# Kernel tuning notes

Hardware: AMD Instinct MI355X
Metric: run time of the kernel (lower is better)

## Reference

```python
import jax, jax.numpy as jnp
import numpy as np

ALPHA = 0.2  # LeakyReLU negative slope
NEG_INF = -9e15


def setup_inputs() -> dict:
    key = jax.random.key(0)
    k1, k2, k3, k4 = jax.random.split(key, 4)
    N, Fin, Fout = 8192, 256, 64
    h = jax.random.normal(k1, (N, Fin), dtype=jnp.float32)
    adj = jax.random.randint(k2, (N, N), 0, 2, dtype=jnp.int32)
    # xavier_uniform with gain=1.414
    def xavier(k, shape, gain=1.414):
        fan_in, fan_out = shape[0], shape[1]
        bound = gain * np.sqrt(6.0 / (fan_in + fan_out))
        return jax.random.uniform(k, shape, jnp.float32, -bound, bound)
    W = xavier(k3, (Fin, Fout))
    a = xavier(k4, (2 * Fout, 1))
    return {"h": h, "adj": adj, "W": W, "a": a}


def reference(h, adj, W, a):
    Fout = W.shape[1]
    Wh = h @ W                                  # [N, Fout]
    Wh1 = Wh @ a[:Fout, :]                      # [N, 1]
    Wh2 = Wh @ a[Fout:, :]                      # [N, 1]
    e = jax.nn.leaky_relu(Wh1 + Wh2.T, negative_slope=ALPHA)  # [N, N]
    attention = jnp.where(adj > 0, e, NEG_INF)
    attention = jax.nn.softmax(attention, axis=1)
    h_prime = attention @ Wh                    # [N, Fout]
    return jax.nn.elu(h_prime)
```

## Files before the change

### kernel.cpp

```cpp
#include <hip/hip_runtime.h>
#include <hip/hip_bf16.h>
#include <math.h>

#define NN 8192
#define FIN 256
#define FOUT 64
#define LRELU_ALPHA 0.2f
#define TI 16
#define TJ 256
#define JS 8
#define JCHUNK (NN / JS)

typedef __attribute__((ext_vector_type(8))) short short8v;
typedef __attribute__((ext_vector_type(4))) float f32x4;

static __device__ inline unsigned short f2bf(float f) {
  __hip_bfloat16 b = __float2bfloat16(f);
  return *reinterpret_cast<unsigned short*>(&b);
}


__global__ __launch_bounds__(256) void gat_prep(
    const float* __restrict__ W, const float* __restrict__ a,
    unsigned short* __restrict__ WF, float* __restrict__ wa1,
    float* __restrict__ wa2) {
  const int t = threadIdx.x;
  if (blockIdx.x < 8) {
    const int wid = blockIdx.x * 4 + (t >> 6);
    const int ks = wid >> 2, nt = wid & 3;
    const int l = t & 63;
    const int kg = l >> 4, nn = l & 15;
    unsigned short frag[8];
#pragma unroll
    for (int e = 0; e < 8; ++e) {
      frag[e] = f2bf(W[(ks * 32 + kg * 8 + e) * FOUT + nt * 16 + nn]);
    }
    *(short8v*)&WF[wid * 512 + l * 8] = *(short8v*)frag;
  } else {
    float s1 = 0.f, s2 = 0.f;
#pragma unroll 4
    for (int c = 0; c < FOUT; c += 4) {
      const float4 wv = *(const float4*)&W[t * FOUT + c];
      const float4 a1 = *(const float4*)&a[c];
      const float4 a2 = *(const float4*)&a[FOUT + c];
      s1 += wv.x * a1.x + wv.y * a1.y + wv.z * a1.z + wv.w * a1.w;
      s2 += wv.x * a2.x + wv.y * a2.y + wv.z * a2.z + wv.w * a2.w;
    }
    wa1[t] = s1;
    wa2[t] = s2;
  }
}

__global__ __launch_bounds__(256) void gat_wh5(
    const float* __restrict__ h, const unsigned short* __restrict__ WF,
    const float* __restrict__ wa1, const float* __restrict__ wa2,
    unsigned short* __restrict__ WhF, float* __restrict__ Wh1,
    float* __restrict__ Wh2) {
  __shared__ __align__(16) float hs[TI][260];

  const int t = threadIdx.x;
  const int i0 = blockIdx.x * TI;

#pragma unroll
  for (int q = 0; q < 4; ++q) {
    const int idx = q * 256 + t;
    const float4 v = *(const float4*)&h[(size_t)i0 * FIN + (size_t)idx * 4];
    const int row = idx >> 6, col = (idx & 63) * 4;
    *(float4*)&hs[row][col] = v;
  }
  __syncthreads();

  {
    const int row = t >> 4, s = t & 15;
    float p1 = 0.f, p2 = 0.f;
#pragma unroll
    for (int q = 0; q < 16; ++q) {
      const int k = s + q * 16;
      const float hv = hs[row][k];
      p1 = fmaf(hv, wa1[k], p1);
      p2 = fmaf(hv, wa2[k], p2);
    }
#pragma unroll
    for (int off = 8; off; off >>= 1) {
      p1 += __shfl_xor(p1, off);
      p2 += __shfl_xor(p2, off);
    }
    if (s == 0) {
      Wh1[i0 + row] = p1;
      Wh2[i0 + row] = p2;
    }
  }

  const int w = t >> 6, l = t & 63;
  const int kg = l >> 4, m = l & 15;
  f32x4 acc = {0.f, 0.f, 0.f, 0.f};
#pragma unroll
  for (int ks = 0; ks < 8; ++ks) {
    const float4 fa = *(const float4*)&hs[m][ks * 32 + kg * 8];
    const float4 fb = *(const float4*)&hs[m][ks * 32 + kg * 8 + 4];
    unsigned short af[8];
    af[0] = f2bf(fa.x); af[1] = f2bf(fa.y);
    af[2] = f2bf(fa.z); af[3] = f2bf(fa.w);
    af[4] = f2bf(fb.x); af[5] = f2bf(fb.y);
    af[6] = f2bf(fb.z); af[7] = f2bf(fb.w);
    const short8v bf = *(const short8v*)&WF[(ks * 4 + w) * 512 + l * 8];
    acc =
        __builtin_amdgcn_mfma_f32_16x16x32_bf16(*(short8v*)af, bf, acc, 0, 0, 0);
  }

  const int k0 = i0 + kg * 4;
  const int col = w * 16 + m;
  const int basef = ((k0 >> 5) * 4 + (col >> 4)) * 512 +
                    (((k0 >> 3) & 3) * 16 + (col & 15)) * 8 + (k0 & 7);
  ushort4 st;
  st.x = f2bf(acc[0]);
  st.y = f2bf(acc[1]);
  st.z = f2bf(acc[2]);
  st.w = f2bf(acc[3]);
  *(ushort4*)&WhF[basef] = st;
}

__global__ __launch_bounds__(256) void gat_attn6(
    const int* __restrict__ adj, const unsigned short* __restrict__ WhF,
    const float* __restrict__ Wh1, const float* __restrict__ Wh2,
    float* __restrict__ num, float* __restrict__ den) {
  __shared__ __align__(16) unsigned short p_lds[2][TI * TJ];
  __shared__ float den_lds[TI];

  const int t = threadIdx.x;
  const int jsplit = blockIdx.x & (JS - 1);
  const int i0 = (blockIdx.x >> 3) * TI;
  const int j0 = jsplit * JCHUNK;

  const int r0 = t >> 5;
  const int col8 = (t & 31) * 8;
  const float w1_0 = Wh1[i0 + r0];
  const float w1_1 = Wh1[i0 + r0 + 8];

  const int w = t >> 6;
  const int l = t & 63;
  const int arow = l & 15;
  const int kg = l >> 4;
  const int colw = w * 16 + arow;

  float ds0 = 0.f, ds1 = 0.f;
  f32x4 acc = {0.f, 0.f, 0.f, 0.f};

  const int wkt = (t & 31) >> 2, wkg = t & 3, wsw = t & 15;
  const int wr0 = wkt * 1024 + wkg * 256 + (((r0 ^ wsw) & 15) << 4);
  const int wr1 = wr0 ^ 128;

  int4 a00, a01, a10, a11;
  float4 w2a, w2b;
  {
    const int4* ap0 = (const int4*)&adj[(size_t)(i0 + r0) * NN + j0 + col8];
    const int4* ap1 = (const int4*)&adj[(size_t)(i0 + r0 + 8) * NN + j0 + col8];
    a00 = ap0[0]; a01 = ap0[1];
    a10 = ap1[0]; a11 = ap1[1];
    w2a = *(const float4*)&Wh2[j0 + col8];
    w2b = *(const float4*)&Wh2[j0 + col8 + 4];
  }

  for (int jb = j0, it = 0; jb < j0 + JCHUNK; jb += TJ, ++it) {
    unsigned short* pl = &p_lds[it & 1][0];

    const float w2v[8] = {w2a.x, w2a.y, w2a.z, w2a.w,
                          w2b.x, w2b.y, w2b.z, w2b.w};
    const int am0[8] = {a00.x, a00.y, a00.z, a00.w, a01.x, a01.y, a01.z, a01.w};
    const int am1[8] = {a10.x, a10.y, a10.z, a10.w, a11.x, a11.y, a11.z, a11.w};

    short8v pv0, pv1;
#pragma unroll
    for (int e = 0; e < 8; ++e) {
      float v0 = w1_0 + w2v[e];
      v0 = v0 > 0.f ? v0 : LRELU_ALPHA * v0;
      float p0 = (am0[e] > 0) ? __expf(v0) : 0.f;
      ds0 += p0;
      pv0[e] = (short)f2bf(p0);
      float v1 = w1_1 + w2v[e];
      v1 = v1 > 0.f ? v1 : LRELU_ALPHA * v1;
      float p1 = (am1[e] > 0) ? __expf(v1) : 0.f;
      ds1 += p1;
      pv1[e] = (short)f2bf(p1);
    }
    *(short8v*)((char*)pl + wr0) = pv0;
    *(short8v*)((char*)pl + wr1) = pv1;

    if (jb + TJ < j0 + JCHUNK) {
      const int jn = jb + TJ;
      const int4* ap0 = (const int4*)&adj[(size_t)(i0 + r0) * NN + jn + col8];
      const int4* ap1 =
          (const int4*)&adj[(size_t)(i0 + r0 + 8) * NN + jn + col8];
      a00 = ap0[0]; a01 = ap0[1];
      a10 = ap1[0]; a11 = ap1[1];
      w2a = *(const float4*)&Wh2[jn + col8];
      w2b = *(const float4*)&Wh2[jn + col8 + 4];
    }

    asm volatile("s_waitcnt lgkmcnt(0)" ::: "memory");
    __builtin_amdgcn_sched_barrier(0);
    __builtin_amdgcn_s_barrier();

    const int kblk0 = jb >> 5;
#pragma unroll
    for (int kt = 0; kt < 8; ++kt) {
      const int swk = (kt * 4 + kg) & 15;
      const int raddr = kt * 1024 + (kg << 8) + ((arow ^ swk) << 4);
      short8v af = *(const short8v*)((const char*)pl + raddr);
      short8v bf = *(const short8v*)&WhF[((kblk0 + kt) * 4 + w) * 512 + l * 8];
      acc = __builtin_amdgcn_mfma_f32_16x16x32_bf16(af, bf, acc, 0, 0, 0);
    }
  }

#pragma unroll
  for (int off = 16; off; off >>= 1) {
    ds0 += __shfl_xor(ds0, off);
    ds1 += __shfl_xor(ds1, off);
  }
  if ((t & 31) == 0) {
    const int rr = t >> 5;
    den_lds[rr] = ds0;
    den_lds[rr + 8] = ds1;
  }
  __syncthreads();
  if (t < TI) den[(size_t)jsplit * NN + i0 + t] = den_lds[t];

#pragma unroll
  for (int r = 0; r < 4; ++r) {
    num[((size_t)jsplit * NN + i0 + kg * 4 + r) * FOUT + colw] = acc[r];
  }
}

__global__ __launch_bounds__(256) void gat_comb(
    const float* __restrict__ num, const float* __restrict__ den,
    float* __restrict__ out) {
  const int idx = blockIdx.x * 256 + threadIdx.x;
  const int row = idx >> 6;
  float n = 0.f, d = 0.f;
#pragma unroll
  for (int s = 0; s < JS; ++s) {
    n += num[(size_t)s * NN * FOUT + idx];
    d += den[(size_t)s * NN + row];
  }
  float v = n / d;
  out[idx] = v > 0.f ? v : expm1f(v);
}

extern "C" void kernel_launch(void* const* d_in, const int* in_sizes, int n_in,
                              void* d_out, int out_size, void* d_ws,
                              size_t ws_size, hipStream_t stream) {
  const float* h = (const float*)d_in[0];
  const int* adj = (const int*)d_in[1];
  const float* W = (const float*)d_in[2];
  const float* a = (const float*)d_in[3];
  float* out = (float*)d_out;

  unsigned short* WhF = (unsigned short*)d_ws;
  float* Wh1 = (float*)((char*)d_ws + (1 << 20));
  float* Wh2 = Wh1 + NN;
  float* num = Wh2 + NN;
  float* den = num + (size_t)JS * NN * FOUT;
  unsigned short* WF = (unsigned short*)((char*)d_ws + (24u << 20));
  float* wa1 = (float*)((char*)d_ws + (24u << 20) + (64u << 10));
  float* wa2 = wa1 + FIN;

  gat_prep<<<9, 256, 0, stream>>>(W, a, WF, wa1, wa2);
  gat_wh5<<<NN / TI, 256, 0, stream>>>(h, WF, wa1, wa2, WhF, Wh1, Wh2);
  gat_attn6<<<(NN / TI) * JS, 256, 0, stream>>>(adj, WhF, Wh1, Wh2, num, den);
  gat_comb<<<NN * FOUT / 256, 256, 0, stream>>>(num, den, out);
}
```

Baseline: 80.19 us.

## Factor exp of LeakyReLU into per-node exponentials and fuse prep into Wh kernel

Precomputes exp(Wh1), exp(0.2*Wh1), exp(Wh2) and exp(0.2*Wh2) per node, so the attention inner loop forms each score as a product of two exponentials instead of evaluating an exp per pair. The sign test becomes a check of whether the product exceeds 1. The W fragment packing and W·a projection are folded into the Wh kernel, where every block recomputes them into shared memory, removing one launch. The cost is twice the Wh2-side loads per tile, redundant per-block prep work, and possible float overflow or underflow in the products, since no max subtraction is applied.

```diff
diff --git a/kernel.cpp b/kernel.cpp
--- a/kernel.cpp
+++ b/kernel.cpp
@@ -5,7 +5,6 @@
 #define NN 8192
 #define FIN 256
 #define FOUT 64
-#define LRELU_ALPHA 0.2f
 #define TI 16
 #define TJ 256
 #define JS 8
@@ -20,23 +19,43 @@
 }
 
 
-__global__ __launch_bounds__(256) void gat_prep(
-    const float* __restrict__ W, const float* __restrict__ a,
-    unsigned short* __restrict__ WF, float* __restrict__ wa1,
-    float* __restrict__ wa2) {
+__global__ __launch_bounds__(256) void gat_wh7(
+    const float* __restrict__ h, const float* __restrict__ W,
+    const float* __restrict__ a, unsigned short* __restrict__ WhF,
+    float* __restrict__ E1, float* __restrict__ F1, float* __restrict__ E2,
+    float* __restrict__ F2) {
+  __shared__ __align__(16) float hs[TI][260];
+  __shared__ __align__(16) unsigned short wfl[16384];
+  __shared__ float wal[2][FIN];
+
   const int t = threadIdx.x;
-  if (blockIdx.x < 8) {
-    const int wid = blockIdx.x * 4 + (t >> 6);
+  const int i0 = blockIdx.x * TI;
+
+#pragma unroll
+  for (int q = 0; q < 4; ++q) {
+    const int idx = q * 256 + t;
+    const float4 v = *(const float4*)&h[(size_t)i0 * FIN + (size_t)idx * 4];
+    const int row = idx >> 6, col = (idx & 63) * 4;
+    *(float4*)&hs[row][col] = v;
+  }
+
+  {
+    const int wid = t >> 3;
     const int ks = wid >> 2, nt = wid & 3;
-    const int l = t & 63;
-    const int kg = l >> 4, nn = l & 15;
-    unsigned short frag[8];
-#pragma unroll
-    for (int e = 0; e < 8; ++e) {
-      frag[e] = f2bf(W[(ks * 32 + kg * 8 + e) * FOUT + nt * 16 + nn]);
-    }
-    *(short8v*)&WF[wid * 512 + l * 8] = *(short8v*)frag;
-  } else {
+#pragma unroll
+    for (int li = 0; li < 8; ++li) {
+      const int l = (t & 7) * 8 + li;
+      const int kg = l >> 4, nn = l & 15;
+      unsigned short fr[8];
+#pragma unroll
+      for (int e = 0; e < 8; ++e) {
+        fr[e] = f2bf(W[(ks * 32 + kg * 8 + e) * FOUT + nt * 16 + nn]);
+      }
+      *(short8v*)&wfl[wid * 512 + l * 8] = *(short8v*)fr;
+    }
+  }
+
+  {
     float s1 = 0.f, s2 = 0.f;
 #pragma unroll 4
     for (int c = 0; c < FOUT; c += 4) {
@@ -46,27 +65,8 @@
       s1 += wv.x * a1.x + wv.y * a1.y + wv.z * a1.z + wv.w * a1.w;
       s2 += wv.x * a2.x + wv.y * a2.y + wv.z * a2.z + wv.w * a2.w;
     }
-    wa1[t] = s1;
-    wa2[t] = s2;
-  }
-}
-
-__global__ __launch_bounds__(256) void gat_wh5(
-    const float* __restrict__ h, const unsigned short* __restrict__ WF,
-    const float* __restrict__ wa1, const float* __restrict__ wa2,
-    unsigned short* __restrict__ WhF, float* __restrict__ Wh1,
-    float* __restrict__ Wh2) {
-  __shared__ __align__(16) float hs[TI][260];
-
-  const int t = threadIdx.x;
-  const int i0 = blockIdx.x * TI;
-
-#pragma unroll
-  for (int q = 0; q < 4; ++q) {
-    const int idx = q * 256 + t;
-    const float4 v = *(const float4*)&h[(size_t)i0 * FIN + (size_t)idx * 4];
-    const int row = idx >> 6, col = (idx & 63) * 4;
-    *(float4*)&hs[row][col] = v;
+    wal[0][t] = s1;
+    wal[1][t] = s2;
   }
   __syncthreads();
 
@@ -77,8 +77,8 @@
     for (int q = 0; q < 16; ++q) {
       const int k = s + q * 16;
       const float hv = hs[row][k];
-      p1 = fmaf(hv, wa1[k], p1);
-      p2 = fmaf(hv, wa2[k], p2);
+      p1 = fmaf(hv, wal[0][k], p1);
+      p2 = fmaf(hv, wal[1][k], p2);
     }
 #pragma unroll
     for (int off = 8; off; off >>= 1) {
@@ -86,8 +86,10 @@
       p2 += __shfl_xor(p2, off);
     }
     if (s == 0) {
-      Wh1[i0 + row] = p1;
-      Wh2[i0 + row] = p2;
+      E1[i0 + row] = __expf(p1);
+      F1[i0 + row] = __expf(0.2f * p1);
+      E2[i0 + row] = __expf(p2);
+      F2[i0 + row] = __expf(0.2f * p2);
     }
   }
 
@@ -103,7 +105,7 @@
     af[2] = f2bf(fa.z); af[3] = f2bf(fa.w);
     af[4] = f2bf(fb.x); af[5] = f2bf(fb.y);
     af[6] = f2bf(fb.z); af[7] = f2bf(fb.w);
-    const short8v bf = *(const short8v*)&WF[(ks * 4 + w) * 512 + l * 8];
+    const short8v bf = *(const short8v*)&wfl[(ks * 4 + w) * 512 + l * 8];
     acc =
         __builtin_amdgcn_mfma_f32_16x16x32_bf16(*(short8v*)af, bf, acc, 0, 0, 0);
   }
@@ -120,9 +122,10 @@
   *(ushort4*)&WhF[basef] = st;
 }
 
-__global__ __launch_bounds__(256) void gat_attn6(
+__global__ __launch_bounds__(256) void gat_attn7(
     const int* __restrict__ adj, const unsigned short* __restrict__ WhF,
-    const float* __restrict__ Wh1, const float* __restrict__ Wh2,
+    const float* __restrict__ E1, const float* __restrict__ F1,
+    const float* __restrict__ E2, const float* __restrict__ F2,
     float* __restrict__ num, float* __restrict__ den) {
   __shared__ __align__(16) unsigned short p_lds[2][TI * TJ];
   __shared__ float den_lds[TI];
@@ -134,8 +137,8 @@
 
   const int r0 = t >> 5;
   const int col8 = (t & 31) * 8;
-  const float w1_0 = Wh1[i0 + r0];
-  const float w1_1 = Wh1[i0 + r0 + 8];
+  const float e1_0 = E1[i0 + r0], f1_0 = F1[i0 + r0];
+  const float e1_1 = E1[i0 + r0 + 8], f1_1 = F1[i0 + r0 + 8];
 
   const int w = t >> 6;
   const int l = t & 63;
@@ -151,35 +154,41 @@
   const int wr1 = wr0 ^ 128;
 
   int4 a00, a01, a10, a11;
-  float4 w2a, w2b;
+  float4 e2a, e2b, f2a, f2b;
   {
     const int4* ap0 = (const int4*)&adj[(size_t)(i0 + r0) * NN + j0 + col8];
     const int4* ap1 = (const int4*)&adj[(size_t)(i0 + r0 + 8) * NN + j0 + col8];
     a00 = ap0[0]; a01 = ap0[1];
     a10 = ap1[0]; a11 = ap1[1];
-    w2a = *(const float4*)&Wh2[j0 + col8];
-    w2b = *(const float4*)&Wh2[j0 + col8 + 4];
+    e2a = *(const float4*)&E2[j0 + col8];
+    e2b = *(const float4*)&E2[j0 + col8 + 4];
+    f2a = *(const float4*)&F2[j0 + col8];
+    f2b = *(const float4*)&F2[j0 + col8 + 4];
   }
 
   for (int jb = j0, it = 0; jb < j0 + JCHUNK; jb += TJ, ++it) {
     unsigned short* pl = &p_lds[it & 1][0];
 
-    const float w2v[8] = {w2a.x, w2a.y, w2a.z, w2a.w,
-                          w2b.x, w2b.y, w2b.z, w2b.w};
+    const float e2v[8] = {e2a.x, e2a.y, e2a.z, e2a.w,
+                          e2b.x, e2b.y, e2b.z, e2b.w};
+    const float f2v[8] = {f2a.x, f2a.y, f2a.z, f2a.w,
+                          f2b.x, f2b.y, f2b.z, f2b.w};
     const int am0[8] = {a00.x, a00.y, a00.z, a00.w, a01.x, a01.y, a01.z, a01.w};
     const int am1[8] = {a10.x, a10.y, a10.z, a10.w, a11.x, a11.y, a11.z, a11.w};
 
     short8v pv0, pv1;
 #pragma unroll
     for (int e = 0; e < 8; ++e) {
-      float v0 = w1_0 + w2v[e];
-      v0 = v0 > 0.f ? v0 : LRELU_ALPHA * v0;
-      float p0 = (am0[e] > 0) ? __expf(v0) : 0.f;
+      const float pE0 = e1_0 * e2v[e];
+      const float pF0 = f1_0 * f2v[e];
+      float p0 = pE0 > 1.f ? pE0 : pF0;
+      p0 = (am0[e] > 0) ? p0 : 0.f;
       ds0 += p0;
       pv0[e] = (short)f2bf(p0);
-      float v1 = w1_1 + w2v[e];
-      v1 = v1 > 0.f ? v1 : LRELU_ALPHA * v1;
-      float p1 = (am1[e] > 0) ? __expf(v1) : 0.f;
+      const float pE1 = e1_1 * e2v[e];
+      const float pF1 = f1_1 * f2v[e];
+      float p1 = pE1 > 1.f ? pE1 : pF1;
+      p1 = (am1[e] > 0) ? p1 : 0.f;
       ds1 += p1;
       pv1[e] = (short)f2bf(p1);
     }
@@ -193,8 +202,10 @@
           (const int4*)&adj[(size_t)(i0 + r0 + 8) * NN + jn + col8];
       a00 = ap0[0]; a01 = ap0[1];
       a10 = ap1[0]; a11 = ap1[1];
-      w2a = *(const float4*)&Wh2[jn + col8];
-      w2b = *(const float4*)&Wh2[jn + col8 + 4];
+      e2a = *(const float4*)&E2[jn + col8];
+      e2b = *(const float4*)&E2[jn + col8 + 4];
+      f2a = *(const float4*)&F2[jn + col8];
+      f2b = *(const float4*)&F2[jn + col8 + 4];
     }
 
     asm volatile("s_waitcnt lgkmcnt(0)" ::: "memory");
@@ -256,16 +267,15 @@
   float* out = (float*)d_out;
 
   unsigned short* WhF = (unsigned short*)d_ws;
-  float* Wh1 = (float*)((char*)d_ws + (1 << 20));
-  float* Wh2 = Wh1 + NN;
-  float* num = Wh2 + NN;
+  float* E1 = (float*)((char*)d_ws + (1 << 20));
+  float* F1 = E1 + NN;
+  float* E2 = F1 + NN;
+  float* F2 = E2 + NN;
+  float* num = (float*)((char*)d_ws + (2 << 20));
   float* den = num + (size_t)JS * NN * FOUT;
-  unsigned short* WF = (unsigned short*)((char*)d_ws + (24u << 20));
-  float* wa1 = (float*)((char*)d_ws + (24u << 20) + (64u << 10));
-  float* wa2 = wa1 + FIN;
-
-  gat_prep<<<9, 256, 0, stream>>>(W, a, WF, wa1, wa2);
-  gat_wh5<<<NN / TI, 256, 0, stream>>>(h, WF, wa1, wa2, WhF, Wh1, Wh2);
-  gat_attn6<<<(NN / TI) * JS, 256, 0, stream>>>(adj, WhF, Wh1, Wh2, num, den);
+
+  gat_wh7<<<NN / TI, 256, 0, stream>>>(h, W, a, WhF, E1, F1, E2, F2);
+  gat_attn7<<<(NN / TI) * JS, 256, 0, stream>>>(adj, WhF, E1, F1, E2, F2, num,
+                                                den);
   gat_comb<<<NN * FOUT / 256, 256, 0, stream>>>(num, den, out);
 }
```

Measured after the change: 89.86 us. 12.1% more time.
